# Optimization experiments

Measured on AMD Instinct MI355X. Metric: run time of the kernel, lower is better.

The kernel has to match this reference:

```python
import jax, jax.numpy as jnp
import numpy as np
from jax import lax

B, D, H, W = 16, 256, 64, 64
P = 8  # patchsize
EPS = 1e-5


def setup_inputs() -> dict:
    key = jax.random.key(0)
    ks = jax.random.split(key, 8)
    s = 0.02
    return {
        "x": jax.random.normal(ks[0], (B, D, H, W), jnp.float32),
        "wq": jax.random.normal(ks[1], (D, D), jnp.float32) * s,
        "bq": jnp.zeros((D,), jnp.float32),
        "wk": jax.random.normal(ks[2], (D, D), jnp.float32) * s,
        "bk": jnp.zeros((D,), jnp.float32),
        "wv": jax.random.normal(ks[3], (D, D), jnp.float32) * s,
        "bv": jnp.zeros((D,), jnp.float32),
        "w_out": jax.random.normal(ks[4], (D, D, 3, 3), jnp.float32) * s,
        "b_out": jnp.zeros((D,), jnp.float32),
        "gamma": jnp.ones((D,), jnp.float32),
        "beta": jnp.zeros((D,), jnp.float32),
        "bn_mean": jnp.zeros((D,), jnp.float32),
        "bn_var": jnp.ones((D,), jnp.float32),
    }


def _conv1x1(x, w, b):
    # x: [b,c,h,w], w: [o,c] (1x1 conv) -> [b,o,h,w]
    return jnp.einsum('bchw,oc->bohw', x, w) + b[None, :, None, None]


def _to_patches(t, p):
    # [b,d,h,w] -> [b, p*p, d*hh*ww]  (matches view+permute(0,2,4,1,3,5)+view)
    b, d, h, w = t.shape
    hh, ww = h // p, w // p
    t = t.reshape(b, d, p, hh, p, ww).transpose(0, 2, 4, 1, 3, 5)
    return t.reshape(b, p * p, d * hh * ww)


def reference(x, wq, bq, wk, bk, wv, bv, w_out, b_out, gamma, beta, bn_mean, bn_var):
    b, d, h, w = x.shape
    p = P
    hh, ww = h // p, w // p

    q = _to_patches(_conv1x1(x, wq, bq), p)  # [b, p^2, d*hh*ww]
    k = _to_patches(_conv1x1(x, wk, bk), p)
    v = _to_patches(_conv1x1(x, wv, bv), p)

    scale = 1.0 / jnp.sqrt(jnp.asarray(q.shape[-1], q.dtype))
    scores = jnp.einsum('bqe,bke->bqk', q, k) * scale  # [b, p^2, p^2]
    attn = jax.nn.softmax(scores, axis=-1)
    out = jnp.einsum('bqk,bke->bqe', attn, v)  # [b, p^2, d*hh*ww]

    # [b,p,p,d,hh,ww] -> permute(0,3,1,4,2,5) -> [b,d,h,w]
    out = out.reshape(b, p, p, d, hh, ww).transpose(0, 3, 1, 4, 2, 5).reshape(b, d, h, w)

    # 3x3 conv, padding 1
    y = lax.conv_general_dilated(out, w_out, window_strides=(1, 1),
                                 padding=((1, 1), (1, 1)),
                                 dimension_numbers=('NCHW', 'OIHW', 'NCHW'))
    y = y + b_out[None, :, None, None]

    # BatchNorm2d (eval mode with running stats)
    inv = gamma / jnp.sqrt(bn_var + EPS)
    y = (y - bn_mean[None, :, None, None]) * inv[None, :, None, None] + beta[None, :, None, None]

    # LeakyReLU(0.2)
    return jnp.where(y >= 0, y, 0.2 * y)
```

## Files before the change

### kernel.cpp

```cpp
#include <hip/hip_runtime.h>
#include <hip/hip_bf16.h>

#define BB 16
#define SS 4096

typedef __attribute__((ext_vector_type(8))) short short8;
typedef __attribute__((ext_vector_type(4))) float float4v;

__global__ __launch_bounds__(256) void wprep_qkv(
    const float* __restrict__ wq, const float* __restrict__ wk,
    const float* __restrict__ wv, __hip_bfloat16* __restrict__ blob) {
  int chunk = blockIdx.x * 256 + threadIdx.x;
  int lane = chunk & 63;
  int ob = (chunk >> 6) & 15;
  int cb = (chunk >> 10) & 7;
  int which = chunk >> 13;
  const float* W = (which == 0) ? wq : (which == 1) ? wk : wv;
  int o = ob * 16 + (lane & 15);
  int c0 = cb * 32 + (lane >> 4) * 8;
  const float* p = W + o * 256 + c0;
  union { uint4 u; __hip_bfloat16 h[8]; } t;
#pragma unroll
  for (int j = 0; j < 8; ++j) t.h[j] = __float2bfloat16(p[j]);
  *reinterpret_cast<uint4*>(blob + (size_t)chunk * 8) = t.u;
}

__global__ __launch_bounds__(256) void qkv_mfma(
    const float* __restrict__ x, const __hip_bfloat16* __restrict__ blob,
    const float* __restrict__ bq, const float* __restrict__ bk,
    const float* __restrict__ bv,
    __hip_bfloat16* __restrict__ qb, __hip_bfloat16* __restrict__ kb,
    __hip_bfloat16* __restrict__ vb) {
  __shared__ short ls[8][64 * 40];
  const int b = blockIdx.y;
  const int s0 = blockIdx.x * 64;
  const int tid = threadIdx.x;
  const int wave = tid >> 6, lane = tid & 63;
  const int q = lane >> 4, m = lane & 15;
  const int sl = tid & 63;
  const int cg = tid >> 6;

  for (int cb = 0; cb < 8; ++cb) {
    const float* xp = x + ((size_t)(b * 256 + cb * 32 + cg * 8)) * SS + s0 + sl;
    union { uint4 u; __hip_bfloat16 h[8]; } t;
#pragma unroll
    for (int i = 0; i < 8; ++i)
      t.h[i] = __float2bfloat16(xp[(size_t)i * SS]);
    *reinterpret_cast<uint4*>(&ls[cb][sl * 40 + cg * 8]) = t.u;
  }
  __syncthreads();

  for (int which = 0; which < 3; ++which) {
    const float* bias = (which == 0) ? bq : (which == 1) ? bk : bv;
    float4v acc[4][4] = {};
#pragma unroll
    for (int cb = 0; cb < 8; ++cb) {
      short8 af[4];
#pragma unroll
      for (int of = 0; of < 4; ++of)
        af[of] = *reinterpret_cast<const short8*>(
            blob +
            ((size_t)(((which * 8 + cb) * 16 + wave * 4 + of) * 64 + lane)) * 8);
      short8 xf[4];
#pragma unroll
      for (int sf = 0; sf < 4; ++sf)
        xf[sf] =
            *reinterpret_cast<const short8*>(&ls[cb][(sf * 16 + m) * 40 + q * 8]);
#pragma unroll
      for (int of = 0; of < 4; ++of)
#pragma unroll
        for (int sf = 0; sf < 4; ++sf)
          acc[of][sf] = __builtin_amdgcn_mfma_f32_16x16x32_bf16(
              af[of], xf[sf], acc[of][sf], 0, 0, 0);
    }
    if (which == 2) {
      const int h = s0 >> 6;
#pragma unroll
      for (int of = 0; of < 4; ++of) {
        int o_base = wave * 64 + of * 16 + q * 4;
#pragma unroll
        for (int sf = 0; sf < 4; ++sf) {
          int w = sf * 16 + m;
          union { uint2 u; __hip_bfloat16 hh[4]; } t;
#pragma unroll
          for (int r = 0; r < 4; ++r)
            t.hh[r] = __float2bfloat16(acc[of][sf][r] + bias[o_base + r]);
          *reinterpret_cast<uint2*>(
              vb + ((size_t)((b * 64 + h) * 64 + w)) * 256 + o_base) = t.u;
        }
      }
    } else {
      __hip_bfloat16* outb = (which == 0) ? qb : kb;
#pragma unroll
      for (int of = 0; of < 4; ++of) {
        int o_base = wave * 64 + of * 16 + q * 4;
#pragma unroll
        for (int r = 0; r < 4; ++r) {
          int o = o_base + r;
          float bi = bias[o];
          __hip_bfloat16* op = outb + ((size_t)(b * 256 + o)) * SS + s0 + m;
#pragma unroll
          for (int sf = 0; sf < 4; ++sf)
            op[sf * 16] = __float2bfloat16(acc[of][sf][r] + bi);
        }
      }
    }
  }
}

__global__ __launch_bounds__(256) void scores_mfma(
    const __hip_bfloat16* __restrict__ qb, const __hip_bfloat16* __restrict__ kb,
    float* __restrict__ part) {
  const int b = blockIdx.y;
  const int d0 = blockIdx.x * 16;
  const int tid = threadIdx.x;
  const int wave = tid >> 6, lane = tid & 63;
  const int q = lane >> 4, m = lane & 15;
  const int t = wave * 16 + m;
  const int arow = (t >> 3) * 8;
  const int acol = (t & 7) * 8;
  float4v acc[4] = {};

  for (int dd = 0; dd < 16; ++dd) {
    const int d = d0 + dd;
    const __hip_bfloat16* qp = qb + ((size_t)(b * 256 + d)) * SS;
    const __hip_bfloat16* kp = kb + ((size_t)(b * 256 + d)) * SS;
#pragma unroll
    for (int khalf = 0; khalf < 2; ++khalf) {
      const int oh = khalf * 4 + q;
      short8 af = *reinterpret_cast<const short8*>(
          qp + (arow + oh) * 64 + acol);
      short8 bf[4];
#pragma unroll
      for (int nt = 0; nt < 4; ++nt) {
        int tp = nt * 16 + m;
        bf[nt] = *reinterpret_cast<const short8*>(
            kp + ((tp >> 3) * 8 + oh) * 64 + (tp & 7) * 8);
      }
#pragma unroll
      for (int nt = 0; nt < 4; ++nt)
        acc[nt] = __builtin_amdgcn_mfma_f32_16x16x32_bf16(af, bf[nt], acc[nt],
                                                          0, 0, 0);
    }
  }
  float* pp = part + ((size_t)(blockIdx.x * BB + b)) * 4096;
#pragma unroll
  for (int nt = 0; nt < 4; ++nt)
#pragma unroll
    for (int r = 0; r < 4; ++r)
      pp[(wave * 16 + q * 4 + r) * 64 + nt * 16 + m] = acc[nt][r];
}

__global__ __launch_bounds__(64) void softmax_kernel(
    const float* __restrict__ part, __hip_bfloat16* __restrict__ attnb) {
  const int t = blockIdx.x;
  const int b = blockIdx.y;
  const int lane = threadIdx.x;
  float v = 0.f;
#pragma unroll
  for (int sl = 0; sl < 16; ++sl)
    v += part[((size_t)(sl * BB + b)) * 4096 + t * 64 + lane];
  v *= 0.0078125f;
  float m = v;
#pragma unroll
  for (int off = 32; off >= 1; off >>= 1) m = fmaxf(m, __shfl_xor(m, off));
  float e = __expf(v - m);
  float s = e;
#pragma unroll
  for (int off = 32; off >= 1; off >>= 1) s += __shfl_xor(s, off);
  attnb[(b * 64 + t) * 64 + lane] = __float2bfloat16(e / s);
}

__global__ __launch_bounds__(256) void apply_mfma(
    const __hip_bfloat16* __restrict__ attnb, const __hip_bfloat16* __restrict__ vb,
    __hip_bfloat16* __restrict__ zb) {
  __shared__ short Vs[64][268];
  const int off = blockIdx.x;
  const int b = blockIdx.y;
  const int oh = off >> 3, ow = off & 7;
  const int tid = threadIdx.x;
#pragma unroll
  for (int i = 0; i < 8; ++i) {
    int chunk = i * 256 + tid;
    int tp = chunk >> 5;
    int cg = chunk & 31;
    int hh = (tp >> 3) * 8 + oh;
    int wwp = (tp & 7) * 8 + ow;
    uint4 val = *reinterpret_cast<const uint4*>(
        vb + ((size_t)((b * 64 + hh) * 64 + wwp)) * 256 + cg * 8);
    *reinterpret_cast<uint4*>(&Vs[tp][cg * 8]) = val;
  }
  __syncthreads();
  const int wave = tid >> 6, lane = tid & 63;
  const int q = lane >> 4, m = lane & 15;
  float4v acc[4][4] = {};
#pragma unroll
  for (int ks = 0; ks < 2; ++ks) {
    short8 af[4];
#pragma unroll
    for (int mt = 0; mt < 4; ++mt)
      af[mt] = *reinterpret_cast<const short8*>(
          attnb + (b * 64 + mt * 16 + m) * 64 + ks * 32 + q * 8);
    short8 bf[4];
#pragma unroll
    for (int nt = 0; nt < 4; ++nt) {
      int d = wave * 64 + nt * 16 + m;
      union { short8 v; short s[8]; } t;
#pragma unroll
      for (int j = 0; j < 8; ++j) t.s[j] = Vs[ks * 32 + q * 8 + j][d];
      bf[nt] = t.v;
    }
#pragma unroll
    for (int mt = 0; mt < 4; ++mt)
#pragma unroll
      for (int nt = 0; nt < 4; ++nt)
        acc[mt][nt] = __builtin_amdgcn_mfma_f32_16x16x32_bf16(
            af[mt], bf[nt], acc[mt][nt], 0, 0, 0);
  }
#pragma unroll
  for (int mt = 0; mt < 4; ++mt)
#pragma unroll
    for (int r = 0; r < 4; ++r) {
      int t = mt * 16 + q * 4 + r;
      int h = (t >> 3) * 8 + oh;
      int w = (t & 7) * 8 + ow;
      __hip_bfloat16* base = zb + ((size_t)((b * 64 + h) * 64 + w)) * 256;
#pragma unroll
      for (int nt = 0; nt < 4; ++nt)
        base[wave * 64 + nt * 16 + m] = __float2bfloat16(acc[mt][nt][r]);
    }
}

__global__ __launch_bounds__(256) void wprep(
    const float* __restrict__ wo, __hip_bfloat16* __restrict__ blob) {
  int chunk = blockIdx.x * 256 + threadIdx.x;
  int l = chunk & 63;
  int ob = (chunk >> 6) & 15;
  int cb = (chunk >> 10) & 7;
  int tap = chunk >> 13;
  int o = ob * 16 + (l & 15);
  int c0 = cb * 32 + (l >> 4) * 8;
  union { uint4 u; __hip_bfloat16 h[8]; } t;
#pragma unroll
  for (int j = 0; j < 8; ++j)
    t.h[j] = __float2bfloat16(wo[((size_t)(o * 256 + c0 + j)) * 9 + tap]);
  *reinterpret_cast<uint4*>(blob + (size_t)chunk * 8) = t.u;
}

__global__ __launch_bounds__(256) void conv_mfma(
    const __hip_bfloat16* __restrict__ z, const __hip_bfloat16* __restrict__ blob,
    const float* __restrict__ bo, const float* __restrict__ gm,
    const float* __restrict__ bt, const float* __restrict__ mn,
    const float* __restrict__ vr, float* __restrict__ out) {
  __shared__ short zs[2][3 * 66 * 40];
  const int idx0 = blockIdx.x;
  const int h = (idx0 & 7) * 8 + ((idx0 >> 3) & 7);
  const int b = idx0 >> 6;
  const int tid = threadIdx.x;
  const int wave = tid >> 6, lane = tid & 63;
  const int q = lane >> 4, m = lane & 15;
  float4v acc[4][4] = {};

  int s_r[4], s_wp[4], s_cg[4];
  bool s_ok[4], s_act[4];
  const __hip_bfloat16* s_base[4];
#pragma unroll
  for (int k = 0; k < 4; ++k) {
    int idx = tid + k * 256;
    bool act = idx < 792;
    int cg = idx & 3;
    int t2 = idx >> 2;
    int wpos = act ? (t2 % 66) : 0;
    int r = act ? (t2 / 66) : 0;
    int h_in = h - 1 + r;
    int w_in = wpos - 1;
    bool ok = act && h_in >= 0 && h_in < 64 && w_in >= 0 && w_in < 64;
    if (!act) { r = 0; wpos = 0; cg = 0; }
    s_r[k] = r; s_wp[k] = wpos; s_cg[k] = cg;
    s_ok[k] = ok; s_act[k] = act;
    s_base[k] = z + ((size_t)((b * 64 + h_in) * 64 + w_in)) * 256 + cg * 8;
  }

  uint4 pf[4];
#pragma unroll
  for (int k = 0; k < 4; ++k)
    pf[k] = s_ok[k] ? *reinterpret_cast<const uint4*>(s_base[k])
                    : make_uint4(0u, 0u, 0u, 0u);
#pragma unroll
  for (int k = 0; k < 4; ++k)
    if (s_act[k])
      *reinterpret_cast<uint4*>(
          &zs[0][(s_r[k] * 66 + s_wp[k]) * 40 + s_cg[k] * 8]) = pf[k];

  short8 wfb[2][4];
#pragma unroll
  for (int of = 0; of < 4; ++of)
    wfb[0][of] = *reinterpret_cast<const short8*>(
        blob + ((size_t)((0 * 16 + wave * 4 + of) * 64 + lane)) * 8);
  __syncthreads();

#pragma unroll 2
  for (int cb = 0; cb < 8; ++cb) {
    const short* cur = zs[cb & 1];
    short* nxt = zs[(cb + 1) & 1];
    if (cb < 7) {
#pragma unroll
      for (int k = 0; k < 4; ++k)
        pf[k] = s_ok[k] ? *reinterpret_cast<const uint4*>(
                              s_base[k] + (size_t)(cb + 1) * 32)
                        : make_uint4(0u, 0u, 0u, 0u);
    }
#pragma unroll
    for (int tap = 0; tap < 9; ++tap) {
      const int kh = tap / 3, kw = tap % 3;
      const int p = (cb + tap) & 1;
      {
        const int ntap = (tap == 8) ? 0 : tap + 1;
        const int ncb = (tap == 8) ? cb + 1 : cb;
        if (ncb < 8) {
#pragma unroll
          for (int of = 0; of < 4; ++of)
            wfb[p ^ 1][of] = *reinterpret_cast<const short8*>(
                blob +
                ((size_t)(((ntap * 8 + ncb) * 16 + wave * 4 + of) * 64 + lane)) *
                    8);
        }
      }
      short8 zf[4];
#pragma unroll
      for (int wfi = 0; wfi < 4; ++wfi) {
        int wpos = wfi * 16 + m + kw;
        zf[wfi] = *reinterpret_cast<const short8*>(
            &cur[(kh * 66 + wpos) * 40 + q * 8]);
      }
#pragma unroll
      for (int of = 0; of < 4; ++of)
#pragma unroll
        for (int wfi = 0; wfi < 4; ++wfi)
          acc[of][wfi] = __builtin_amdgcn_mfma_f32_16x16x32_bf16(
              wfb[p][of], zf[wfi], acc[of][wfi], 0, 0, 0);
    }
    if (cb < 7) {
#pragma unroll
      for (int k = 0; k < 4; ++k)
        if (s_act[k])
          *reinterpret_cast<uint4*>(
              &nxt[(s_r[k] * 66 + s_wp[k]) * 40 + s_cg[k] * 8]) = pf[k];
    }
    __syncthreads();
  }
#pragma unroll
  for (int of = 0; of < 4; ++of) {
    int o_base = wave * 64 + of * 16 + q * 4;
#pragma unroll
    for (int r = 0; r < 4; ++r) {
      int o = o_base + r;
      float sc = gm[o] * rsqrtf(vr[o] + 1e-5f);
      float sh = bt[o] + (bo[o] - mn[o]) * sc;
#pragma unroll
      for (int wfi = 0; wfi < 4; ++wfi) {
        float y = acc[of][wfi][r] * sc + sh;
        y = (y >= 0.f) ? y : 0.2f * y;
        out[(((size_t)(b * 256 + o)) * 64 + h) * 64 + wfi * 16 + m] = y;
      }
    }
  }
}

extern "C" void kernel_launch(void* const* d_in, const int* in_sizes, int n_in,
                              void* d_out, int out_size, void* d_ws,
                              size_t ws_size, hipStream_t stream) {
  (void)in_sizes; (void)n_in; (void)out_size; (void)ws_size;
  const float* x  = (const float*)d_in[0];
  const float* wq = (const float*)d_in[1];
  const float* bq = (const float*)d_in[2];
  const float* wk = (const float*)d_in[3];
  const float* bk = (const float*)d_in[4];
  const float* wv = (const float*)d_in[5];
  const float* bv = (const float*)d_in[6];
  const float* wo = (const float*)d_in[7];
  const float* bo = (const float*)d_in[8];
  const float* gm = (const float*)d_in[9];
  const float* bt = (const float*)d_in[10];
  const float* mn = (const float*)d_in[11];
  const float* vr = (const float*)d_in[12];
  float* out = (float*)d_out;

  char* ws = (char*)d_ws;
  __hip_bfloat16* qb = (__hip_bfloat16*)(ws);
  __hip_bfloat16* kb = (__hip_bfloat16*)(ws + 33554432);
  __hip_bfloat16* attnb = (__hip_bfloat16*)(ws + 67371008);
  __hip_bfloat16* blob = (__hip_bfloat16*)(ws + 67502080);
  __hip_bfloat16* vb = (__hip_bfloat16*)d_out;
  __hip_bfloat16* blob_a = (__hip_bfloat16*)((char*)d_out + 33554432);
  float* part = (float*)((char*)d_out + 37748736);

  wprep<<<288, 256, 0, stream>>>(wo, blob);
  wprep_qkv<<<96, 256, 0, stream>>>(wq, wk, wv, blob_a);
  qkv_mfma<<<dim3(64, BB), 256, 0, stream>>>(x, blob_a, bq, bk, bv,
                                             qb, kb, vb);
  scores_mfma<<<dim3(16, BB), 256, 0, stream>>>(qb, kb, part);
  softmax_kernel<<<dim3(64, BB), 64, 0, stream>>>(part, attnb);
  apply_mfma<<<dim3(64, BB), 256, 0, stream>>>(attnb, vb, qb );
  conv_mfma<<<dim3(BB * 64), 256, 0, stream>>>(qb, blob, bo, gm, bt, mn, vr,
                                               out);
}
```

Before: 352.6 us.

## Split QKV projection across grid z and deepen conv weight prefetch

The QKV projection kernel now launches one block per output (q, k or v) along grid z instead of looping over all three in one block. Each block restages its x tile through a single small LDS buffer per channel block rather than holding all channels. This triples parallelism and cuts LDS use, which should raise occupancy, but x is read and converted three times and each channel step adds two barriers. Separately, the 3x3 conv kernel now prefetches weight fragments two taps ahead through a three-slot register ring instead of one tap ahead, which costs more registers.

```diff
diff --git a/kernel.cpp b/kernel.cpp
--- a/kernel.cpp
+++ b/kernel.cpp
@@ -31,78 +31,75 @@
     const float* __restrict__ bv,
     __hip_bfloat16* __restrict__ qb, __hip_bfloat16* __restrict__ kb,
     __hip_bfloat16* __restrict__ vb) {
-  __shared__ short ls[8][64 * 40];
+  __shared__ short ls[64 * 40];
+  const int which = blockIdx.z;
   const int b = blockIdx.y;
   const int s0 = blockIdx.x * 64;
+  const float* bias = (which == 0) ? bq : (which == 1) ? bk : bv;
+  __hip_bfloat16* outb = (which == 0) ? qb : kb;
   const int tid = threadIdx.x;
   const int wave = tid >> 6, lane = tid & 63;
   const int q = lane >> 4, m = lane & 15;
   const int sl = tid & 63;
   const int cg = tid >> 6;
+  float4v acc[4][4] = {};
 
   for (int cb = 0; cb < 8; ++cb) {
-    const float* xp = x + ((size_t)(b * 256 + cb * 32 + cg * 8)) * SS + s0 + sl;
-    union { uint4 u; __hip_bfloat16 h[8]; } t;
-#pragma unroll
-    for (int i = 0; i < 8; ++i)
-      t.h[i] = __float2bfloat16(xp[(size_t)i * SS]);
-    *reinterpret_cast<uint4*>(&ls[cb][sl * 40 + cg * 8]) = t.u;
-  }
-  __syncthreads();
-
-  for (int which = 0; which < 3; ++which) {
-    const float* bias = (which == 0) ? bq : (which == 1) ? bk : bv;
-    float4v acc[4][4] = {};
-#pragma unroll
-    for (int cb = 0; cb < 8; ++cb) {
-      short8 af[4];
-#pragma unroll
-      for (int of = 0; of < 4; ++of)
-        af[of] = *reinterpret_cast<const short8*>(
-            blob +
-            ((size_t)(((which * 8 + cb) * 16 + wave * 4 + of) * 64 + lane)) * 8);
-      short8 xf[4];
+    __syncthreads();
+    {
+      const float* xp = x + ((size_t)(b * 256 + cb * 32 + cg * 8)) * SS + s0 + sl;
+      union { uint4 u; __hip_bfloat16 h[8]; } t;
+#pragma unroll
+      for (int i = 0; i < 8; ++i)
+        t.h[i] = __float2bfloat16(xp[(size_t)i * SS]);
+      *reinterpret_cast<uint4*>(&ls[sl * 40 + cg * 8]) = t.u;
+    }
+    __syncthreads();
+    short8 af[4];
+#pragma unroll
+    for (int of = 0; of < 4; ++of)
+      af[of] = *reinterpret_cast<const short8*>(
+          blob +
+          ((size_t)(((which * 8 + cb) * 16 + wave * 4 + of) * 64 + lane)) * 8);
+    short8 xf[4];
+#pragma unroll
+    for (int sf = 0; sf < 4; ++sf)
+      xf[sf] = *reinterpret_cast<const short8*>(&ls[(sf * 16 + m) * 40 + q * 8]);
+#pragma unroll
+    for (int of = 0; of < 4; ++of)
 #pragma unroll
       for (int sf = 0; sf < 4; ++sf)
-        xf[sf] =
-            *reinterpret_cast<const short8*>(&ls[cb][(sf * 16 + m) * 40 + q * 8]);
-#pragma unroll
-      for (int of = 0; of < 4; ++of)
+        acc[of][sf] = __builtin_amdgcn_mfma_f32_16x16x32_bf16(
+            af[of], xf[sf], acc[of][sf], 0, 0, 0);
+  }
+  if (which == 2) {
+    const int h = s0 >> 6;
+#pragma unroll
+    for (int of = 0; of < 4; ++of) {
+      int o_base = wave * 64 + of * 16 + q * 4;
+#pragma unroll
+      for (int sf = 0; sf < 4; ++sf) {
+        int w = sf * 16 + m;
+        union { uint2 u; __hip_bfloat16 hh[4]; } t;
+#pragma unroll
+        for (int r = 0; r < 4; ++r)
+          t.hh[r] = __float2bfloat16(acc[of][sf][r] + bias[o_base + r]);
+        *reinterpret_cast<uint2*>(
+            vb + ((size_t)((b * 64 + h) * 64 + w)) * 256 + o_base) = t.u;
+      }
+    }
+  } else {
+#pragma unroll
+    for (int of = 0; of < 4; ++of) {
+      int o_base = wave * 64 + of * 16 + q * 4;
+#pragma unroll
+      for (int r = 0; r < 4; ++r) {
+        int o = o_base + r;
+        float bi = bias[o];
+        __hip_bfloat16* op = outb + ((size_t)(b * 256 + o)) * SS + s0 + m;
 #pragma unroll
         for (int sf = 0; sf < 4; ++sf)
-          acc[of][sf] = __builtin_amdgcn_mfma_f32_16x16x32_bf16(
-              af[of], xf[sf], acc[of][sf], 0, 0, 0);
-    }
-    if (which == 2) {
-      const int h = s0 >> 6;
-#pragma unroll
-      for (int of = 0; of < 4; ++of) {
-        int o_base = wave * 64 + of * 16 + q * 4;
-#pragma unroll
-        for (int sf = 0; sf < 4; ++sf) {
-          int w = sf * 16 + m;
-          union { uint2 u; __hip_bfloat16 hh[4]; } t;
-#pragma unroll
-          for (int r = 0; r < 4; ++r)
-            t.hh[r] = __float2bfloat16(acc[of][sf][r] + bias[o_base + r]);
-          *reinterpret_cast<uint2*>(
-              vb + ((size_t)((b * 64 + h) * 64 + w)) * 256 + o_base) = t.u;
-        }
-      }
-    } else {
-      __hip_bfloat16* outb = (which == 0) ? qb : kb;
-#pragma unroll
-      for (int of = 0; of < 4; ++of) {
-        int o_base = wave * 64 + of * 16 + q * 4;
-#pragma unroll
-        for (int r = 0; r < 4; ++r) {
-          int o = o_base + r;
-          float bi = bias[o];
-          __hip_bfloat16* op = outb + ((size_t)(b * 256 + o)) * SS + s0 + m;
-#pragma unroll
-          for (int sf = 0; sf < 4; ++sf)
-            op[sf * 16] = __float2bfloat16(acc[of][sf][r] + bi);
-        }
+          op[sf * 16] = __float2bfloat16(acc[of][sf][r] + bi);
       }
     }
   }
@@ -292,11 +289,15 @@
       *reinterpret_cast<uint4*>(
           &zs[0][(s_r[k] * 66 + s_wp[k]) * 40 + s_cg[k] * 8]) = pf[k];
 
-  short8 wfb[2][4];
+  short8 wfb[3][4];
 #pragma unroll
   for (int of = 0; of < 4; ++of)
     wfb[0][of] = *reinterpret_cast<const short8*>(
-        blob + ((size_t)((0 * 16 + wave * 4 + of) * 64 + lane)) * 8);
+        blob + ((size_t)(((0 * 8 + 0) * 16 + wave * 4 + of) * 64 + lane)) * 8);
+#pragma unroll
+  for (int of = 0; of < 4; ++of)
+    wfb[1][of] = *reinterpret_cast<const short8*>(
+        blob + ((size_t)(((1 * 8 + 0) * 16 + wave * 4 + of) * 64 + lane)) * 8);
   __syncthreads();
 
 #pragma unroll 2
@@ -313,16 +314,16 @@
 #pragma unroll
     for (int tap = 0; tap < 9; ++tap) {
       const int kh = tap / 3, kw = tap % 3;
-      const int p = (cb + tap) & 1;
       {
-        const int ntap = (tap == 8) ? 0 : tap + 1;
-        const int ncb = (tap == 8) ? cb + 1 : cb;
-        if (ncb < 8) {
+        int ft = tap + 2;
+        int fcb = cb;
+        if (ft >= 9) { ft -= 9; fcb = cb + 1; }
+        if (fcb < 8) {
 #pragma unroll
           for (int of = 0; of < 4; ++of)
-            wfb[p ^ 1][of] = *reinterpret_cast<const short8*>(
+            wfb[(tap + 2) % 3][of] = *reinterpret_cast<const short8*>(
                 blob +
-                ((size_t)(((ntap * 8 + ncb) * 16 + wave * 4 + of) * 64 + lane)) *
+                ((size_t)(((ft * 8 + fcb) * 16 + wave * 4 + of) * 64 + lane)) *
                     8);
         }
       }
@@ -338,7 +339,7 @@
 #pragma unroll
         for (int wfi = 0; wfi < 4; ++wfi)
           acc[of][wfi] = __builtin_amdgcn_mfma_f32_16x16x32_bf16(
-              wfb[p][of], zf[wfi], acc[of][wfi], 0, 0, 0);
+              wfb[tap % 3][of], zf[wfi], acc[of][wfi], 0, 0, 0);
     }
     if (cb < 7) {
 #pragma unroll
@@ -397,8 +398,8 @@
 
   wprep<<<288, 256, 0, stream>>>(wo, blob);
   wprep_qkv<<<96, 256, 0, stream>>>(wq, wk, wv, blob_a);
-  qkv_mfma<<<dim3(64, BB), 256, 0, stream>>>(x, blob_a, bq, bk, bv,
-                                             qb, kb, vb);
+  qkv_mfma<<<dim3(64, BB, 3), 256, 0, stream>>>(x, blob_a, bq, bk, bv,
+                                                qb, kb, vb);
   scores_mfma<<<dim3(16, BB), 256, 0, stream>>>(qb, kb, part);
   softmax_kernel<<<dim3(64, BB), 64, 0, stream>>>(part, attnb);
   apply_mfma<<<dim3(64, BB), 256, 0, stream>>>(attnb, vb, qb );
```

Result: slower. 417.4 us (+18.4%).
